# Optimization experiments

Measured on AMD Instinct MI355X. Metric: run time of the kernel, lower is better.

The kernel has to match this reference:

```python
import jax, jax.numpy as jnp
import numpy as np

HEADS = 8
DIM_HEAD = 64
DIM = 512
INNER = HEADS * DIM_HEAD  # 512
SCALE = DIM_HEAD ** -0.5


def setup_inputs() -> dict:
    key = jax.random.key(0)
    k1, k2, k3, k4 = jax.random.split(key, 4)
    B, N = 2, 4096
    x = jax.random.normal(k1, (B, N, DIM), dtype=jnp.float32)
    # nn.Linear(dim, inner*3, bias=False): weight [3*inner, dim]; y = x @ W.T
    w_qkv = jax.random.normal(k2, (3 * INNER, DIM), dtype=jnp.float32) * (DIM ** -0.5)
    w_out = jax.random.normal(k3, (DIM, INNER), dtype=jnp.float32) * (INNER ** -0.5)
    b_out = jax.random.normal(k4, (DIM,), dtype=jnp.float32) * 0.01
    return {"x": x, "w_qkv": w_qkv, "w_out": w_out, "b_out": b_out, "H": 64, "W": 64}


def reference(x, w_qkv, w_out, b_out, H, W):
    B, N, _ = x.shape
    qkv = jnp.einsum('bnd,ed->bne', x, w_qkv)  # [B, N, 3*inner]
    q, k, v = jnp.split(qkv, 3, axis=-1)
    def to_heads(t):
        return t.reshape(B, N, HEADS, DIM_HEAD).transpose(0, 2, 1, 3)  # b h n d
    q, k, v = to_heads(q), to_heads(k), to_heads(v)
    dots = jnp.einsum('bhid,bhjd->bhij', q, k) * SCALE
    attn = jax.nn.softmax(dots, axis=-1)  # dropout p=0.0 -> identity
    out = jnp.einsum('bhij,bhjd->bhid', attn, v)
    out = out.transpose(0, 2, 1, 3).reshape(B, N, INNER)
    return jnp.einsum('bne,de->bnd', out, w_out) + b_out
```

## Files before the change

kernel.cpp:

```cpp
#include <hip/hip_runtime.h>
#include <hip/hip_bf16.h>

typedef __hip_bfloat16 bf16;
typedef __attribute__((ext_vector_type(8))) short short8;
typedef __attribute__((ext_vector_type(4))) short shortx4;
typedef __attribute__((ext_vector_type(4))) float floatx4;
typedef __attribute__((ext_vector_type(4))) int intx4;

#define MFMA16(a, b, c) __builtin_amdgcn_mfma_f32_16x16x32_bf16((a), (b), (c), 0, 0, 0)
#define EXP2(x) __builtin_amdgcn_exp2f(x)

__device__ __forceinline__ short f2s(float v) {
    return __builtin_bit_cast(short, __float2bfloat16(v));
}

__device__ __forceinline__ int packhi(float lo, float hi) {
    return (int)__builtin_amdgcn_perm(__builtin_bit_cast(unsigned, hi),
                                      __builtin_bit_cast(unsigned, lo),
                                      0x07060302u);
}

__device__ __forceinline__ short8 cvt8v(float4 f0, float4 f1) {
    short8 r;
    r[0] = f2s(f0.x); r[1] = f2s(f0.y); r[2] = f2s(f0.z); r[3] = f2s(f0.w);
    r[4] = f2s(f1.x); r[5] = f2s(f1.y); r[6] = f2s(f1.z); r[7] = f2s(f1.w);
    return r;
}

__device__ __forceinline__ int swz(int row, int chunk) {
    return row * 64 + ((chunk ^ (row & 7)) << 3);
}

__global__ __launch_bounds__(256) void cvt_inputs(
    const float* __restrict__ x, const float* __restrict__ wq,
    const float* __restrict__ wo, bf16* __restrict__ xb,
    bf16* __restrict__ wqb, bf16* __restrict__ wob)
{
    int idx = blockIdx.x * 256 + threadIdx.x;
    const float* src;
    bf16* dst;
    int off;
    if (idx < 524288)      { src = x;  dst = xb;  off = idx; }
    else if (idx < 622592) { src = wq; dst = wqb; off = idx - 524288; }
    else                   { src = wo; dst = wob; off = idx - 622592; }
    float4 f0 = ((const float4*)src)[off * 2];
    float4 f1 = ((const float4*)src)[off * 2 + 1];
    *(short8*)&((short*)dst)[off * 8] = cvt8v(f0, f1);
}

__global__ __launch_bounds__(256) void qkv_gemm(
    const bf16* __restrict__ xb, const bf16* __restrict__ wqb,
    bf16* __restrict__ q, bf16* __restrict__ k, bf16* __restrict__ vt)
{
    __shared__ short pool[20480];
    short (*As)[128][40] = (short(*)[128][40])pool;
    short (*Bs)[128][40] = (short(*)[128][40])(pool + 10240);
    short (*Qt)[144] = (short(*)[144])pool;
    short (*Vt)[136] = (short(*)[136])pool;
    const int t = threadIdx.x;
    const int bm = blockIdx.x * 128;
    const int be = blockIdx.y * 128;
    const int w = t >> 6, lane = t & 63, lq = lane >> 4, lm = lane & 15;
    const int wr = w >> 1, wc = w & 1;
    const int srow = t >> 1, scol = (t & 1) * 16;
    const float C = 0.18033688011112042f;

    const bf16* xp = &xb[(size_t)(bm + srow) * 512 + scol];
    const bf16* wp = &wqb[(size_t)(be + srow) * 512 + scol];

    intx4 xr[2], wr4[2];
    auto issue = [&](int k0) {
        xr[0] = *(const intx4*)(xp + k0);
        xr[1] = *(const intx4*)(xp + k0 + 8);
        wr4[0] = *(const intx4*)(wp + k0);
        wr4[1] = *(const intx4*)(wp + k0 + 8);
    };
    auto commit = [&](int buf) {
        *(intx4*)&As[buf][srow][scol]     = xr[0];
        *(intx4*)&As[buf][srow][scol + 8] = xr[1];
        *(intx4*)&Bs[buf][srow][scol]     = wr4[0];
        *(intx4*)&Bs[buf][srow][scol + 8] = wr4[1];
    };

    floatx4 acc[4][4];
#pragma unroll
    for (int i = 0; i < 4; ++i)
#pragma unroll
        for (int j = 0; j < 4; ++j) acc[i][j] = {0.f, 0.f, 0.f, 0.f};

    issue(0);
    commit(0);
    __syncthreads();
    int cur = 0;
    for (int k0 = 0; k0 < 512; k0 += 32) {
        const bool more = (k0 + 32) < 512;
        if (more) issue(k0 + 32);
        short8 af[4], bf[4];
#pragma unroll
        for (int mt = 0; mt < 4; ++mt) af[mt] = *(const short8*)&As[cur][wr * 64 + mt * 16 + lm][lq * 8];
#pragma unroll
        for (int nt = 0; nt < 4; ++nt) bf[nt] = *(const short8*)&Bs[cur][wc * 64 + nt * 16 + lm][lq * 8];
#pragma unroll
        for (int mt = 0; mt < 4; ++mt)
#pragma unroll
            for (int nt = 0; nt < 4; ++nt)
                acc[mt][nt] = MFMA16(af[mt], bf[nt], acc[mt][nt]);
        if (more) {
            commit(cur ^ 1);
            __syncthreads();
        }
        cur ^= 1;
    }

    const int which = be >> 9;
    __syncthreads();
    if (which < 2) {
        const float scale = (which == 0) ? C : 1.0f;
#pragma unroll
        for (int nt = 0; nt < 4; ++nt) {
            const int e_loc = wc * 64 + nt * 16 + lm;
#pragma unroll
            for (int mt = 0; mt < 4; ++mt)
#pragma unroll
                for (int r = 0; r < 4; ++r)
                    Qt[wr * 64 + mt * 16 + lq * 4 + r][e_loc] = f2s(acc[mt][nt][r] * scale);
        }
        __syncthreads();
        bf16* dst = (which == 0) ? q : k;
        const int tr = t >> 1, th = t & 1;
        const int grow = bm + tr;
        const int b = grow >> 12, n = grow & 4095;
        const int h = ((be + th * 64) & 511) >> 6;
        bf16* p = dst + ((size_t)(b * 8 + h) * 4096 + n) * 64;
#pragma unroll
        for (int c = 0; c < 8; ++c)
            *(intx4*)&p[c * 8] = *(const intx4*)&Qt[tr][th * 64 + c * 8];
    } else {
#pragma unroll
        for (int nt = 0; nt < 4; ++nt) {
            const int e_loc = wc * 64 + nt * 16 + lm;
#pragma unroll
            for (int mt = 0; mt < 4; ++mt) {
                const int col = wr * 64 + 4 * (mt & 1) + 8 * lq + 32 * (mt >> 1);
                shortx4 v4;
#pragma unroll
                for (int r = 0; r < 4; ++r) v4[r] = f2s(acc[mt][nt][r]);
                *(shortx4*)&Vt[e_loc][col] = v4;
            }
        }
        __syncthreads();
        const int b = bm >> 12, n0 = bm & 4095;
        const int h0 = (be - 1024) >> 6;
        const int row = t >> 1, cb = (t & 1) * 64;
        const int h = h0 + (row >> 6), d = row & 63;
        const size_t gb = ((size_t)(b * 8 + h) * 64 + d) * 4096 + n0 + cb;
#pragma unroll
        for (int c = 0; c < 8; ++c)
            *(intx4*)&vt[gb + c * 8] = *(const intx4*)&Vt[row][cb + c * 8];
    }
}

__global__ __launch_bounds__(256, 2) void flash_attn(
    const bf16* __restrict__ q, const bf16* __restrict__ k,
    const bf16* __restrict__ vt, bf16* __restrict__ out)
{
    __shared__ short pool[24576];
    short* Qs = pool;
    short* Ks0 = pool + 8192;
    short* Vs0 = pool + 16384;
    const int t = threadIdx.x;
    const int n = blockIdx.x;
    const int L = (n & 7) * 64 + (n >> 3);
    const int i0 = (L & 31) * 128;
    const int bh = L >> 5;
    const int w = t >> 6, lane = t & 63, lq = lane >> 4, lm = lane & 15;
    const int h = w >> 1;
    const int par = w & 1;
    const floatx4 zero4 = {0.f, 0.f, 0.f, 0.f};

    const size_t nbase = (size_t)bh * 4096 * 64;
    const size_t vbase = (size_t)bh * 64 * 4096;
    const int r0 = t >> 3, ch = t & 7;

#pragma unroll
    for (int it = 0; it < 4; ++it) {
        int row = it * 32 + r0;
        *(intx4*)&Qs[swz(row, ch)] =
            *(const intx4*)&q[nbase + (size_t)(i0 + row) * 64 + ch * 8];
    }

    intx4 kreg[2], vreg[2];
    auto issue = [&](int j0n) {
        kreg[0] = *(const intx4*)&k[nbase + (size_t)(j0n + r0) * 64 + ch * 8];
        kreg[1] = *(const intx4*)&k[nbase + (size_t)(j0n + 32 + r0) * 64 + ch * 8];
        vreg[0] = *(const intx4*)&vt[vbase + (size_t)r0 * 4096 + j0n + ch * 8];
        vreg[1] = *(const intx4*)&vt[vbase + (size_t)(32 + r0) * 4096 + j0n + ch * 8];
    };
    auto commit = [&](int buf) {
        short* Kb = Ks0 + buf * 4096;
        short* Vb = Vs0 + buf * 4096;
        *(intx4*)&Kb[swz(r0, ch)]      = kreg[0];
        *(intx4*)&Kb[swz(32 + r0, ch)] = kreg[1];
        *(intx4*)&Vb[swz(r0, ch)]      = vreg[0];
        *(intx4*)&Vb[swz(32 + r0, ch)] = vreg[1];
    };

    issue(0);
    commit(0);
    __syncthreads();

    short8 aq0[4], aq1[4];
#pragma unroll
    for (int g = 0; g < 4; ++g) {
        const int qrow = h * 64 + g * 16 + lm;
        aq0[g] = *(const short8*)&Qs[swz(qrow, lq)];
        aq1[g] = *(const short8*)&Qs[swz(qrow, 4 + lq)];
    }

    float l_lane[4] = {0.f, 0.f, 0.f, 0.f};
    floatx4 o_acc[4][4];
#pragma unroll
    for (int g = 0; g < 4; ++g)
#pragma unroll
        for (int dt = 0; dt < 4; ++dt) o_acc[g][dt] = zero4;

    const int jtb = par * 2;
    int cur = 0;
    for (int j0 = 0; j0 < 4096; j0 += 64) {
        const bool more = (j0 + 64) < 4096;
        if (more) issue(j0 + 64);
        const short* Kb = Ks0 + cur * 4096;
        const short* Vb = Vs0 + cur * 4096;

        intx4 pk[4];
#pragma unroll
        for (int q2 = 0; q2 < 2; ++q2) {
            const int krow = (jtb + q2) * 16 + lm;
            short8 bk0 = *(const short8*)&Kb[swz(krow, lq)];
            short8 bk1 = *(const short8*)&Kb[swz(krow, 4 + lq)];
#pragma unroll
            for (int g = 0; g < 4; ++g) {
                floatx4 s4 = MFMA16(bk0, aq0[g], zero4);
                s4 = MFMA16(bk1, aq1[g], s4);
                float e0 = EXP2(s4[0]);
                float e1 = EXP2(s4[1]);
                float e2 = EXP2(s4[2]);
                float e3 = EXP2(s4[3]);
                l_lane[g] += (e0 + e1) + (e2 + e3);
                pk[g][q2 * 2]     = packhi(e0, e1);
                pk[g][q2 * 2 + 1] = packhi(e2, e3);
            }
        }

#pragma unroll
        for (int dt = 0; dt < 4; ++dt) {
            const int vrow = dt * 16 + lm;
            short8 av = *(const short8*)&Vb[swz(vrow, par * 4 + lq)];
#pragma unroll
            for (int g = 0; g < 4; ++g)
                o_acc[g][dt] = MFMA16(av, __builtin_bit_cast(short8, pk[g]), o_acc[g][dt]);
        }

        if (more) {
            commit(cur ^ 1);
            __syncthreads();
        }
        cur ^= 1;
    }

    __syncthreads();
    float* Red = (float*)(pool + 8192);
    float* Lx  = (float*)pool;
    if (par == 1) {
#pragma unroll
        for (int g = 0; g < 4; ++g) {
            Lx[h * 256 + g * 64 + lane] = l_lane[g];
#pragma unroll
            for (int dt = 0; dt < 4; ++dt)
#pragma unroll
                for (int r = 0; r < 4; ++r)
                    Red[h * 4096 + ((g * 4 + dt) * 4 + r) * 64 + lane] = o_acc[g][dt][r];
        }
    }
    __syncthreads();
    if (par == 0) {
        const int b = bh >> 3, hd = bh & 7;
        short* Os = pool + 1024 + h * 1024;
        const int il = lane >> 2, cc = (lane & 3) * 16;
#pragma unroll
        for (int g = 0; g < 4; ++g) {
            float l = l_lane[g] + Lx[h * 256 + g * 64 + lane];
#pragma unroll
            for (int dt = 0; dt < 4; ++dt)
#pragma unroll
                for (int r = 0; r < 4; ++r)
                    o_acc[g][dt][r] += Red[h * 4096 + ((g * 4 + dt) * 4 + r) * 64 + lane];
            l += __shfl_xor(l, 16);
            l += __shfl_xor(l, 32);
            const float inv_l = 1.0f / l;
#pragma unroll
            for (int dt = 0; dt < 4; ++dt)
#pragma unroll
                for (int r = 0; r < 4; ++r)
                    Os[lm * 64 + dt * 16 + lq * 4 + r] = f2s(o_acc[g][dt][r] * inv_l);
            const int i = i0 + h * 64 + g * 16 + il;
            intx4 v0 = *(const intx4*)&Os[il * 64 + cc];
            intx4 v1 = *(const intx4*)&Os[il * 64 + cc + 8];
            *(intx4*)&out[((size_t)b * 4096 + i) * 512 + hd * 64 + cc] = v0;
            *(intx4*)&out[((size_t)b * 4096 + i) * 512 + hd * 64 + cc + 8] = v1;
        }
    }
}

__global__ __launch_bounds__(256) void out_gemm(
    const bf16* __restrict__ a, const bf16* __restrict__ wob,
    const float* __restrict__ bias, float* __restrict__ y)
{
    __shared__ short As[2][128][40];
    __shared__ short Bs[2][64][40];
    const int t = threadIdx.x;
    const int bm = blockIdx.x * 128;
    const int be = blockIdx.y * 64;
    const int w = t >> 6, lane = t & 63, lq = lane >> 4, lm = lane & 15;
    const int wr = w >> 1, wc = w & 1;
    const int srow = t >> 1, scol = (t & 1) * 16;
    const int brow = t >> 2, bcol = (t & 3) * 8;

    const bf16* ap = &a[(size_t)(bm + srow) * 512 + scol];
    const bf16* wp = &wob[(size_t)(be + brow) * 512 + bcol];

    intx4 ar[2], br;
    auto issue = [&](int k0) {
        ar[0] = *(const intx4*)(ap + k0);
        ar[1] = *(const intx4*)(ap + k0 + 8);
        br    = *(const intx4*)(wp + k0);
    };
    auto commit = [&](int buf) {
        *(intx4*)&As[buf][srow][scol]     = ar[0];
        *(intx4*)&As[buf][srow][scol + 8] = ar[1];
        *(intx4*)&Bs[buf][brow][bcol]     = br;
    };

    floatx4 acc[4][2];
#pragma unroll
    for (int i = 0; i < 4; ++i)
#pragma unroll
        for (int j = 0; j < 2; ++j) acc[i][j] = {0.f, 0.f, 0.f, 0.f};

    issue(0);
    commit(0);
    __syncthreads();
    int cur = 0;
    for (int k0 = 0; k0 < 512; k0 += 32) {
        const bool more = (k0 + 32) < 512;
        if (more) issue(k0 + 32);
        short8 af[4], bf[2];
#pragma unroll
        for (int mt = 0; mt < 4; ++mt) af[mt] = *(const short8*)&As[cur][wr * 64 + mt * 16 + lm][lq * 8];
#pragma unroll
        for (int nt = 0; nt < 2; ++nt) bf[nt] = *(const short8*)&Bs[cur][wc * 32 + nt * 16 + lm][lq * 8];
#pragma unroll
        for (int mt = 0; mt < 4; ++mt)
#pragma unroll
            for (int nt = 0; nt < 2; ++nt)
                acc[mt][nt] = MFMA16(af[mt], bf[nt], acc[mt][nt]);
        if (more) {
            commit(cur ^ 1);
            __syncthreads();
        }
        cur ^= 1;
    }

#pragma unroll
    for (int nt = 0; nt < 2; ++nt) {
        const int gcol = be + wc * 32 + nt * 16 + lm;
        const float bv = bias[gcol];
#pragma unroll
        for (int mt = 0; mt < 4; ++mt) {
#pragma unroll
            for (int r = 0; r < 4; ++r) {
                int grow = bm + wr * 64 + mt * 16 + lq * 4 + r;
                y[(size_t)grow * 512 + gcol] = acc[mt][nt][r] + bv;
            }
        }
    }
}

extern "C" void kernel_launch(void* const* d_in, const int* in_sizes, int n_in,
                              void* d_out, int out_size, void* d_ws, size_t ws_size,
                              hipStream_t stream) {
    const float* x     = (const float*)d_in[0];
    const float* w_qkv = (const float*)d_in[1];
    const float* w_out = (const float*)d_in[2];
    const float* b_out = (const float*)d_in[3];

    const size_t HEAD_ELEMS = (size_t)16 * 4096 * 64;
    bf16* qw  = (bf16*)d_ws;
    bf16* kw  = qw + HEAD_ELEMS;
    bf16* vtw = kw + HEAD_ELEMS;
    bf16* aw  = vtw + HEAD_ELEMS;
    bf16* xb  = aw + HEAD_ELEMS;
    bf16* wqb = xb + (size_t)8192 * 512;
    bf16* wob = wqb + (size_t)1536 * 512;
    float* y  = (float*)d_out;

    cvt_inputs<<<2560, 256, 0, stream>>>(x, w_qkv, w_out, xb, wqb, wob);
    qkv_gemm<<<dim3(64, 12), 256, 0, stream>>>(xb, wqb, qw, kw, vtw);
    flash_attn<<<dim3(512), 256, 0, stream>>>(qw, kw, vtw, aw);
    out_gemm<<<dim3(64, 8), 256, 0, stream>>>(aw, wob, b_out, y);
}
```

Baseline: 189.3 us.

## Split flash attention into 64-row Q tiles with 4-way KV split and direct LDS loads

Flash attention now uses 64-row query tiles per block, doubling the grid to 1024 blocks. Each of the four waves handles a 16-key slice of every 64-key tile and uses the K=16 MFMA for the PV product. K/V tiles are staged with global_load_lds directly into swizzled LDS instead of going through registers, and MFMA sections get raised wave priority. Shared memory shrinks and occupancy is raised to 4 blocks per CU, and the V layout in qkv_gemm gets an extra XOR swizzle to match. The cost is a larger cross-wave reduction of partial O and l through LDS at the end.

```diff
diff --git a/kernel.cpp b/kernel.cpp
--- a/kernel.cpp
+++ b/kernel.cpp
@@ -6,8 +6,10 @@
 typedef __attribute__((ext_vector_type(4))) short shortx4;
 typedef __attribute__((ext_vector_type(4))) float floatx4;
 typedef __attribute__((ext_vector_type(4))) int intx4;
+typedef __attribute__((ext_vector_type(2))) int intx2;
 
 #define MFMA16(a, b, c) __builtin_amdgcn_mfma_f32_16x16x32_bf16((a), (b), (c), 0, 0, 0)
+#define MFMA16K16(a, b, c) __builtin_amdgcn_mfma_f32_16x16x16bf16_1k((a), (b), (c), 0, 0, 0)
 #define EXP2(x) __builtin_amdgcn_exp2f(x)
 
 __device__ __forceinline__ short f2s(float v) {
@@ -29,6 +31,12 @@
 
 __device__ __forceinline__ int swz(int row, int chunk) {
     return row * 64 + ((chunk ^ (row & 7)) << 3);
+}
+
+__device__ __forceinline__ void gload16(const bf16* g, short* l) {
+    __builtin_amdgcn_global_load_lds(
+        (const __attribute__((address_space(1))) void*)g,
+        (__attribute__((address_space(3))) void*)l, 16, 0, 0);
 }
 
 __global__ __launch_bounds__(256) void cvt_inputs(
@@ -139,9 +147,10 @@
 #pragma unroll
         for (int nt = 0; nt < 4; ++nt) {
             const int e_loc = wc * 64 + nt * 16 + lm;
+            const int xd = ((e_loc >> 3) & 1) << 2;
 #pragma unroll
             for (int mt = 0; mt < 4; ++mt) {
-                const int col = wr * 64 + 4 * (mt & 1) + 8 * lq + 32 * (mt >> 1);
+                const int col = (wr * 64 + 4 * (mt & 1) + 8 * lq + 32 * (mt >> 1)) ^ xd;
                 shortx4 v4;
 #pragma unroll
                 for (int r = 0; r < 4; ++r) v4[r] = f2s(acc[mt][nt][r]);
@@ -160,22 +169,21 @@
     }
 }
 
-__global__ __launch_bounds__(256, 2) void flash_attn(
+__global__ __launch_bounds__(256, 4) void flash_attn(
     const bf16* __restrict__ q, const bf16* __restrict__ k,
     const bf16* __restrict__ vt, bf16* __restrict__ out)
 {
-    __shared__ short pool[24576];
+    __shared__ short pool[20480];
     short* Qs = pool;
-    short* Ks0 = pool + 8192;
-    short* Vs0 = pool + 16384;
+    short* Ks0 = pool + 4096;
+    short* Vs0 = pool + 12288;
     const int t = threadIdx.x;
     const int n = blockIdx.x;
-    const int L = (n & 7) * 64 + (n >> 3);
-    const int i0 = (L & 31) * 128;
-    const int bh = L >> 5;
+    const int L = (n & 7) * 128 + (n >> 3);
+    const int i0 = (L & 63) * 64;
+    const int bh = L >> 6;
     const int w = t >> 6, lane = t & 63, lq = lane >> 4, lm = lane & 15;
-    const int h = w >> 1;
-    const int par = w & 1;
+    const int par = w;
     const floatx4 zero4 = {0.f, 0.f, 0.f, 0.f};
 
     const size_t nbase = (size_t)bh * 4096 * 64;
@@ -183,36 +191,31 @@
     const int r0 = t >> 3, ch = t & 7;
 
 #pragma unroll
-    for (int it = 0; it < 4; ++it) {
+    for (int it = 0; it < 2; ++it) {
         int row = it * 32 + r0;
         *(intx4*)&Qs[swz(row, ch)] =
             *(const intx4*)&q[nbase + (size_t)(i0 + row) * 64 + ch * 8];
     }
 
-    intx4 kreg[2], vreg[2];
-    auto issue = [&](int j0n) {
-        kreg[0] = *(const intx4*)&k[nbase + (size_t)(j0n + r0) * 64 + ch * 8];
-        kreg[1] = *(const intx4*)&k[nbase + (size_t)(j0n + 32 + r0) * 64 + ch * 8];
-        vreg[0] = *(const intx4*)&vt[vbase + (size_t)r0 * 4096 + j0n + ch * 8];
-        vreg[1] = *(const intx4*)&vt[vbase + (size_t)(32 + r0) * 4096 + j0n + ch * 8];
+    const int lr0 = w * 8 + (lane >> 3);
+    const int lr1 = 32 + lr0;
+    const int cA = ((lane & 7) ^ (lane >> 3)) * 8;
+    auto stage = [&](int j0n, int buf) {
+        short* Kb = Ks0 + buf * 4096 + w * 512;
+        short* Vb = Vs0 + buf * 4096 + w * 512;
+        gload16(&k[nbase + (size_t)(j0n + lr0) * 64 + cA], Kb);
+        gload16(&k[nbase + (size_t)(j0n + lr1) * 64 + cA], Kb + 2048);
+        gload16(&vt[vbase + (size_t)lr0 * 4096 + j0n + cA], Vb);
+        gload16(&vt[vbase + (size_t)lr1 * 4096 + j0n + cA], Vb + 2048);
     };
-    auto commit = [&](int buf) {
-        short* Kb = Ks0 + buf * 4096;
-        short* Vb = Vs0 + buf * 4096;
-        *(intx4*)&Kb[swz(r0, ch)]      = kreg[0];
-        *(intx4*)&Kb[swz(32 + r0, ch)] = kreg[1];
-        *(intx4*)&Vb[swz(r0, ch)]      = vreg[0];
-        *(intx4*)&Vb[swz(32 + r0, ch)] = vreg[1];
-    };
-
-    issue(0);
-    commit(0);
+
+    stage(0, 0);
     __syncthreads();
 
     short8 aq0[4], aq1[4];
 #pragma unroll
     for (int g = 0; g < 4; ++g) {
-        const int qrow = h * 64 + g * 16 + lm;
+        const int qrow = g * 16 + lm;
         aq0[g] = *(const short8*)&Qs[swz(qrow, lq)];
         aq1[g] = *(const short8*)&Qs[swz(qrow, 4 + lq)];
     }
@@ -224,77 +227,90 @@
 #pragma unroll
         for (int dt = 0; dt < 4; ++dt) o_acc[g][dt] = zero4;
 
-    const int jtb = par * 2;
+    const int krow = par * 16 + lm;
+    const int vpar_hi = (par >> 1) * 4;
+    const int vpar_lo = ((par & 1) ^ ((lm >> 3) & 1)) * 4;
+
     int cur = 0;
     for (int j0 = 0; j0 < 4096; j0 += 64) {
         const bool more = (j0 + 64) < 4096;
-        if (more) issue(j0 + 64);
+        if (more) stage(j0 + 64, cur ^ 1);
         const short* Kb = Ks0 + cur * 4096;
         const short* Vb = Vs0 + cur * 4096;
 
-        intx4 pk[4];
-#pragma unroll
-        for (int q2 = 0; q2 < 2; ++q2) {
-            const int krow = (jtb + q2) * 16 + lm;
-            short8 bk0 = *(const short8*)&Kb[swz(krow, lq)];
-            short8 bk1 = *(const short8*)&Kb[swz(krow, 4 + lq)];
-#pragma unroll
-            for (int g = 0; g < 4; ++g) {
-                floatx4 s4 = MFMA16(bk0, aq0[g], zero4);
-                s4 = MFMA16(bk1, aq1[g], s4);
-                float e0 = EXP2(s4[0]);
-                float e1 = EXP2(s4[1]);
-                float e2 = EXP2(s4[2]);
-                float e3 = EXP2(s4[3]);
-                l_lane[g] += (e0 + e1) + (e2 + e3);
-                pk[g][q2 * 2]     = packhi(e0, e1);
-                pk[g][q2 * 2 + 1] = packhi(e2, e3);
-            }
-        }
-
+        short8 bk0 = *(const short8*)&Kb[swz(krow, lq)];
+        short8 bk1 = *(const short8*)&Kb[swz(krow, 4 + lq)];
+        shortx4 pk[4];
+#pragma unroll
+        for (int g = 0; g < 4; ++g) {
+            floatx4 s4 = MFMA16(bk0, aq0[g], zero4);
+            s4 = MFMA16(bk1, aq1[g], s4);
+            float e0 = EXP2(s4[0]);
+            float e1 = EXP2(s4[1]);
+            float e2 = EXP2(s4[2]);
+            float e3 = EXP2(s4[3]);
+            l_lane[g] += (e0 + e1) + (e2 + e3);
+            intx2 pi2;
+            pi2[0] = packhi(e0, e1);
+            pi2[1] = packhi(e2, e3);
+            pk[g] = __builtin_bit_cast(shortx4, pi2);
+        }
+
+        __builtin_amdgcn_s_setprio(1);
 #pragma unroll
         for (int dt = 0; dt < 4; ++dt) {
             const int vrow = dt * 16 + lm;
-            short8 av = *(const short8*)&Vb[swz(vrow, par * 4 + lq)];
+            shortx4 av = *(const shortx4*)&Vb[swz(vrow, vpar_hi + lq) + vpar_lo];
 #pragma unroll
             for (int g = 0; g < 4; ++g)
-                o_acc[g][dt] = MFMA16(av, __builtin_bit_cast(short8, pk[g]), o_acc[g][dt]);
-        }
-
-        if (more) {
-            commit(cur ^ 1);
-            __syncthreads();
-        }
+                o_acc[g][dt] = MFMA16K16(av, pk[g], o_acc[g][dt]);
+        }
+        __builtin_amdgcn_s_setprio(0);
+
+        if (more) __syncthreads();
         cur ^= 1;
     }
 
     __syncthreads();
-    float* Red = (float*)(pool + 8192);
-    float* Lx  = (float*)pool;
-    if (par == 1) {
-#pragma unroll
-        for (int g = 0; g < 4; ++g) {
-            Lx[h * 256 + g * 64 + lane] = l_lane[g];
-#pragma unroll
-            for (int dt = 0; dt < 4; ++dt)
-#pragma unroll
-                for (int r = 0; r < 4; ++r)
-                    Red[h * 4096 + ((g * 4 + dt) * 4 + r) * 64 + lane] = o_acc[g][dt][r];
-        }
+    float* Red = (float*)pool;
+#pragma unroll
+    for (int gg = 0; gg < 2; ++gg) {
+        if (par) {
+            float* base = Red + (par - 1) * 2048;
+#pragma unroll
+            for (int gi = 0; gi < 2; ++gi)
+#pragma unroll
+                for (int dt = 0; dt < 4; ++dt)
+                    *(floatx4*)&base[(gi * 4 + dt) * 256 + lane * 4] = o_acc[gg * 2 + gi][dt];
+        }
+        __syncthreads();
+        if (par == 0) {
+#pragma unroll
+            for (int p = 0; p < 3; ++p) {
+                float* base = Red + p * 2048;
+#pragma unroll
+                for (int gi = 0; gi < 2; ++gi)
+#pragma unroll
+                    for (int dt = 0; dt < 4; ++dt)
+                        o_acc[gg * 2 + gi][dt] += *(const floatx4*)&base[(gi * 4 + dt) * 256 + lane * 4];
+            }
+        }
+        __syncthreads();
+    }
+    float* Lx = (float*)pool;
+    if (par) {
+#pragma unroll
+        for (int g = 0; g < 4; ++g) Lx[(par - 1) * 256 + g * 64 + lane] = l_lane[g];
     }
     __syncthreads();
     if (par == 0) {
         const int b = bh >> 3, hd = bh & 7;
-        short* Os = pool + 1024 + h * 1024;
+        short* Os = pool + 2048;
         const int il = lane >> 2, cc = (lane & 3) * 16;
 #pragma unroll
         for (int g = 0; g < 4; ++g) {
-            float l = l_lane[g] + Lx[h * 256 + g * 64 + lane];
-#pragma unroll
-            for (int dt = 0; dt < 4; ++dt)
-#pragma unroll
-                for (int r = 0; r < 4; ++r)
-                    o_acc[g][dt][r] += Red[h * 4096 + ((g * 4 + dt) * 4 + r) * 64 + lane];
+            float l = l_lane[g] + Lx[g * 64 + lane] + Lx[256 + g * 64 + lane]
+                                + Lx[512 + g * 64 + lane];
             l += __shfl_xor(l, 16);
             l += __shfl_xor(l, 32);
             const float inv_l = 1.0f / l;
@@ -303,7 +319,7 @@
 #pragma unroll
                 for (int r = 0; r < 4; ++r)
                     Os[lm * 64 + dt * 16 + lq * 4 + r] = f2s(o_acc[g][dt][r] * inv_l);
-            const int i = i0 + h * 64 + g * 16 + il;
+            const int i = i0 + g * 16 + il;
             intx4 v0 = *(const intx4*)&Os[il * 64 + cc];
             intx4 v1 = *(const intx4*)&Os[il * 64 + cc + 8];
             *(intx4*)&out[((size_t)b * 4096 + i) * 512 + hd * 64 + cc] = v0;
@@ -406,6 +422,6 @@
 
     cvt_inputs<<<2560, 256, 0, stream>>>(x, w_qkv, w_out, xb, wqb, wob);
     qkv_gemm<<<dim3(64, 12), 256, 0, stream>>>(xb, wqb, qw, kw, vtw);
-    flash_attn<<<dim3(512), 256, 0, stream>>>(qw, kw, vtw, aw);
+    flash_attn<<<dim3(1024), 256, 0, stream>>>(qw, kw, vtw, aw);
     out_gemm<<<dim3(64, 8), 256, 0, stream>>>(aw, wob, b_out, y);
 }
```

Result: slower. 259.0 us (+36.8%).

## Software-pipeline attention loop: overlap QK of next tile with PV of current

Applied to the files above, without the earlier changes.

Restructures the main attention loop so the QK^T/exp step for tile t+1 runs alongside the PV matmul for tile t. K and V global loads and LDS commits are split and staggered so K for a future tile is written while V of the current tile is still in use. The intent is to raise MFMA utilisation by giving the scheduler independent work and hiding load latency. It costs more live registers (a second pk buffer) and more complex buffer-index logic, which could reduce occupancy or introduce a race.

```diff
diff --git a/kernel.cpp b/kernel.cpp
--- a/kernel.cpp
+++ b/kernel.cpp
@@ -190,49 +190,31 @@
     }
 
     intx4 kreg[2], vreg[2];
-    auto issue = [&](int j0n) {
+    auto issueK = [&](int j0n) {
         kreg[0] = *(const intx4*)&k[nbase + (size_t)(j0n + r0) * 64 + ch * 8];
         kreg[1] = *(const intx4*)&k[nbase + (size_t)(j0n + 32 + r0) * 64 + ch * 8];
+    };
+    auto issueV = [&](int j0n) {
         vreg[0] = *(const intx4*)&vt[vbase + (size_t)r0 * 4096 + j0n + ch * 8];
         vreg[1] = *(const intx4*)&vt[vbase + (size_t)(32 + r0) * 4096 + j0n + ch * 8];
     };
-    auto commit = [&](int buf) {
+    auto commitK = [&](int buf) {
         short* Kb = Ks0 + buf * 4096;
-        short* Vb = Vs0 + buf * 4096;
         *(intx4*)&Kb[swz(r0, ch)]      = kreg[0];
         *(intx4*)&Kb[swz(32 + r0, ch)] = kreg[1];
+    };
+    auto commitV = [&](int buf) {
+        short* Vb = Vs0 + buf * 4096;
         *(intx4*)&Vb[swz(r0, ch)]      = vreg[0];
         *(intx4*)&Vb[swz(32 + r0, ch)] = vreg[1];
     };
 
-    issue(0);
-    commit(0);
-    __syncthreads();
-
     short8 aq0[4], aq1[4];
-#pragma unroll
-    for (int g = 0; g < 4; ++g) {
-        const int qrow = h * 64 + g * 16 + lm;
-        aq0[g] = *(const short8*)&Qs[swz(qrow, lq)];
-        aq1[g] = *(const short8*)&Qs[swz(qrow, 4 + lq)];
-    }
-
     float l_lane[4] = {0.f, 0.f, 0.f, 0.f};
     floatx4 o_acc[4][4];
-#pragma unroll
-    for (int g = 0; g < 4; ++g)
-#pragma unroll
-        for (int dt = 0; dt < 4; ++dt) o_acc[g][dt] = zero4;
-
     const int jtb = par * 2;
-    int cur = 0;
-    for (int j0 = 0; j0 < 4096; j0 += 64) {
-        const bool more = (j0 + 64) < 4096;
-        if (more) issue(j0 + 64);
-        const short* Kb = Ks0 + cur * 4096;
-        const short* Vb = Vs0 + cur * 4096;
-
-        intx4 pk[4];
+
+    auto qk = [&](const short* Kb, intx4* pko) {
 #pragma unroll
         for (int q2 = 0; q2 < 2; ++q2) {
             const int krow = (jtb + q2) * 16 + lm;
@@ -247,25 +229,61 @@
                 float e2 = EXP2(s4[2]);
                 float e3 = EXP2(s4[3]);
                 l_lane[g] += (e0 + e1) + (e2 + e3);
-                pk[g][q2 * 2]     = packhi(e0, e1);
-                pk[g][q2 * 2 + 1] = packhi(e2, e3);
+                pko[g][q2 * 2]     = packhi(e0, e1);
+                pko[g][q2 * 2 + 1] = packhi(e2, e3);
             }
         }
-
+    };
+    auto pv = [&](const short* Vb, const intx4* pki) {
 #pragma unroll
         for (int dt = 0; dt < 4; ++dt) {
             const int vrow = dt * 16 + lm;
             short8 av = *(const short8*)&Vb[swz(vrow, par * 4 + lq)];
 #pragma unroll
             for (int g = 0; g < 4; ++g)
-                o_acc[g][dt] = MFMA16(av, __builtin_bit_cast(short8, pk[g]), o_acc[g][dt]);
-        }
-
-        if (more) {
-            commit(cur ^ 1);
-            __syncthreads();
-        }
-        cur ^= 1;
+                o_acc[g][dt] = MFMA16(av, __builtin_bit_cast(short8, pki[g]), o_acc[g][dt]);
+        }
+    };
+
+    issueK(0); issueV(0);
+    commitK(0); commitV(0);
+    __syncthreads();
+
+#pragma unroll
+    for (int g = 0; g < 4; ++g) {
+        const int qrow = h * 64 + g * 16 + lm;
+        aq0[g] = *(const short8*)&Qs[swz(qrow, lq)];
+        aq1[g] = *(const short8*)&Qs[swz(qrow, 4 + lq)];
+    }
+#pragma unroll
+    for (int g = 0; g < 4; ++g)
+#pragma unroll
+        for (int dt = 0; dt < 4; ++dt) o_acc[g][dt] = zero4;
+
+    issueK(64); issueV(64);
+    intx4 pk[4];
+    qk(Ks0, pk);
+    commitK(1); commitV(1);
+    __syncthreads();
+    issueK(128); issueV(128);
+
+    for (int tt = 0; tt < 64; ++tt) {
+        const int a = tt & 1, b = a ^ 1;
+        if (tt < 62) {
+            commitK(a);
+            if (tt < 61) issueK((tt + 3) * 64);
+        }
+        intx4 pk2[4];
+        if (tt < 63) qk(Ks0 + b * 4096, pk2);
+        pv(Vs0 + a * 4096, pk);
+        __syncthreads();
+        if (tt < 62) {
+            commitV(a);
+            if (tt < 61) issueV((tt + 3) * 64);
+        }
+        if (tt < 63) {
+            pk[0] = pk2[0]; pk[1] = pk2[1]; pk[2] = pk2[2]; pk[3] = pk2[3];
+        }
     }
 
     __syncthreads();
```

New measurement: 186.0 us. No clear change (-1.7%).
